# Kernel tuning notes

Hardware: AMD Instinct MI355X
Metric: run time of the kernel (lower is better)

The kernel has to match this reference:

```python
import jax, jax.numpy as jnp
import numpy as np

N_NODES = 100000
N_EDGES = 3200000
N_FEAT = 16
N_GRAPHS = 1024


def setup_inputs() -> dict:
    key = jax.random.key(0)
    ks = jax.random.split(key, 12)
    x = jax.random.normal(ks[0], (N_NODES, N_FEAT), dtype=jnp.float32)
    edge_index = jax.random.randint(ks[1], (2, N_EDGES), 0, N_NODES, dtype=jnp.int32)
    batch = jnp.sort(jax.random.randint(ks[2], (N_NODES,), 0, N_GRAPHS, dtype=jnp.int32))
    def lin(k, fan_in, fan_out):
        s = 1.0 / np.sqrt(fan_in)
        return jax.random.uniform(k, (fan_in, fan_out), jnp.float32, -s, s)
    W1 = lin(ks[3], N_FEAT, 64); b1 = jnp.zeros((64,), jnp.float32)
    W2 = lin(ks[4], 64, 32);     b2 = jnp.zeros((32,), jnp.float32)
    fc1_W = lin(ks[5], 32, 16);  fc1_b = jnp.zeros((16,), jnp.float32)
    fc2_W = lin(ks[6], 16, 1);   fc2_b = jnp.zeros((1,), jnp.float32)
    return {"x": x, "edge_index": edge_index, "batch": batch,
            "W1": W1, "b1": b1, "W2": W2, "b2": b2,
            "fc1_W": fc1_W, "fc1_b": fc1_b, "fc2_W": fc2_W, "fc2_b": fc2_b}


def _gcn_conv(h, W, b, src, dst, norm, n_nodes):
    # h: [N, Fin] -> [N, Fout]; symmetric-normalized scatter-add (PyG GCNConv)
    h = h @ W
    msg = h[src] * norm[:, None]            # edge-wise gather + scale
    out = jax.ops.segment_sum(msg, dst, num_segments=n_nodes)
    return out + b


def reference(x, edge_index, batch, W1, b1, W2, b2, fc1_W, fc1_b, fc2_W, fc2_b):
    n_nodes = x.shape[0]
    # add self-loops
    loops = jnp.arange(n_nodes, dtype=edge_index.dtype)
    src = jnp.concatenate([edge_index[0], loops])
    dst = jnp.concatenate([edge_index[1], loops])
    deg = jax.ops.segment_sum(jnp.ones_like(dst, dtype=x.dtype), dst, num_segments=n_nodes)
    dinv = jnp.where(deg > 0, jax.lax.rsqrt(deg), 0.0)
    norm = dinv[src] * dinv[dst]

    h = jax.nn.relu(_gcn_conv(x, W1, b1, src, dst, norm, n_nodes))
    # dropout p=0.2 is identity at inference
    h = jax.nn.relu(_gcn_conv(h, W2, b2, src, dst, norm, n_nodes))

    # global mean pool over graphs
    sums = jax.ops.segment_sum(h, batch, num_segments=N_GRAPHS)
    cnts = jax.ops.segment_sum(jnp.ones((n_nodes,), h.dtype), batch, num_segments=N_GRAPHS)
    g = sums / jnp.maximum(cnts, 1.0)[:, None]

    g = jax.nn.relu(g @ fc1_W + fc1_b)
    # dropout p=0.5 is identity at inference
    out = g @ fc2_W + fc2_b
    return jax.nn.sigmoid(out)  # [N_GRAPHS, 1]
```

## Files before the change

### kernel.cpp

```cpp
#include <hip/hip_runtime.h>
#include <math.h>

#define NNODES  100000
#define NEDGES  3200000
#define NGRAPHS 1024
#define BNODES  196
#define NBUCK   ((NNODES + BNODES - 1) / BNODES)
#define SCAP    12288
#define CHUNK   4096
#define NCHUNKS ((NEDGES + CHUNK - 1) / CHUNK)

typedef int iv4 __attribute__((ext_vector_type(4)));
typedef float fv2 __attribute__((ext_vector_type(2)));

#if defined(__has_builtin)
#if __has_builtin(__builtin_amdgcn_cvt_pk_f32_fp8) && __has_builtin(__builtin_amdgcn_cvt_pk_fp8_f32)
#define HW_FP8 1
#endif
#endif

__device__ __forceinline__ unsigned bf16pair(float a, float b) {
    unsigned ua = __float_as_uint(a), ub = __float_as_uint(b);
    ua += 0x7fffu + ((ua >> 16) & 1u);
    ub += 0x7fffu + ((ub >> 16) & 1u);
    return (ua >> 16) | (ub & 0xffff0000u);
}
__device__ __forceinline__ float bflo(unsigned u) { return __uint_as_float(u << 16); }
__device__ __forceinline__ float bfhi(unsigned u) { return __uint_as_float(u & 0xffff0000u); }

__device__ __forceinline__ unsigned fp8_of(float v) {
    unsigned s = (__float_as_uint(v) >> 24) & 0x80u;
    float a = fminf(fabsf(v), 448.f);
    unsigned ub = __float_as_uint(a);
    unsigned lsb = (ub >> 20) & 1u;
    ub += 0x0007FFFFu + lsb;
    int em = (int)(ub >> 20) - (120 << 3);
    if (em < 1) return s;
    if (em > 0x7E) em = 0x7E;
    return s | (unsigned)em;
}
__device__ __forceinline__ float fp8_to_f(unsigned b) {
    unsigned em = b & 0x7Fu;
    unsigned s = (b & 0x80u) << 24;
    float f = __uint_as_float(s | ((em + 0x3C0u) << 20));
    return (em >= 8u) ? f : 0.f;
}
__device__ __forceinline__ void fp8x4_to_f(unsigned w, float& f0, float& f1, float& f2, float& f3) {
#ifdef HW_FP8
    fv2 lo = __builtin_amdgcn_cvt_pk_f32_fp8((int)w, false);
    fv2 hi = __builtin_amdgcn_cvt_pk_f32_fp8((int)w, true);
    f0 = lo.x; f1 = lo.y; f2 = hi.x; f3 = hi.y;
#else
    f0 = fp8_to_f(w & 0xFFu);
    f1 = fp8_to_f((w >> 8) & 0xFFu);
    f2 = fp8_to_f((w >> 16) & 0xFFu);
    f3 = fp8_to_f(w >> 24);
#endif
}
__device__ __forceinline__ unsigned fp8x4_pack(float a, float b, float c, float d) {
    a = fminf(fmaxf(a, -448.f), 448.f);
    b = fminf(fmaxf(b, -448.f), 448.f);
    c = fminf(fmaxf(c, -448.f), 448.f);
    d = fminf(fmaxf(d, -448.f), 448.f);
#ifdef HW_FP8
    int w = __builtin_amdgcn_cvt_pk_fp8_f32(a, b, 0, false);
    w = __builtin_amdgcn_cvt_pk_fp8_f32(c, d, w, true);
    return (unsigned)w;
#else
    return fp8_of(a) | (fp8_of(b) << 8) | (fp8_of(c) << 16) | (fp8_of(d) << 24);
#endif
}


__global__ void zero4_kernel(int4* p, int nvec) {
    int i = blockIdx.x * blockDim.x + threadIdx.x;
    if (i < nvec) p[i] = make_int4(0, 0, 0, 0);
}


__global__ void binA_kernel(const int* __restrict__ src, const int* __restrict__ dst,
                            int* __restrict__ bucketCur, int* __restrict__ stage) {
    __shared__ int lcnt[NBUCK + 1];
    __shared__ int boff[NBUCK + 1];
    __shared__ int gbase[NBUCK + 1];
    __shared__ int cur[NBUCK + 1];
    __shared__ int ssum[256];
    __shared__ int packed[CHUNK];
    __shared__ unsigned short bof[CHUNK];
    int tid = threadIdx.x;
    int beg = blockIdx.x * CHUNK;
    int end = beg + CHUNK; if (end > NEDGES) end = NEDGES;
    int cnt = end - beg;

    for (int i = tid; i <= NBUCK; i += 256) lcnt[i] = 0;
    __syncthreads();

    int ent[16];
    int bk[16];
#pragma unroll
    for (int it = 0; it < 4; ++it) {
        int e0 = beg + tid * 4 + it * 1024;
        if (e0 < end) {
            iv4 d4 = __builtin_nontemporal_load((const iv4*)(dst + e0));
            iv4 s4 = __builtin_nontemporal_load((const iv4*)(src + e0));
            int b;
            b = d4.x / BNODES; ent[it*4+0] = s4.x | ((d4.x - b*BNODES) << 17); bk[it*4+0] = b; atomicAdd(&lcnt[b], 1);
            b = d4.y / BNODES; ent[it*4+1] = s4.y | ((d4.y - b*BNODES) << 17); bk[it*4+1] = b; atomicAdd(&lcnt[b], 1);
            b = d4.z / BNODES; ent[it*4+2] = s4.z | ((d4.z - b*BNODES) << 17); bk[it*4+2] = b; atomicAdd(&lcnt[b], 1);
            b = d4.w / BNODES; ent[it*4+3] = s4.w | ((d4.w - b*BNODES) << 17); bk[it*4+3] = b; atomicAdd(&lcnt[b], 1);
        } else {
            bk[it*4+0] = -1; bk[it*4+1] = -1; bk[it*4+2] = -1; bk[it*4+3] = -1;
            ent[it*4+0] = 0; ent[it*4+1] = 0; ent[it*4+2] = 0; ent[it*4+3] = 0;
        }
    }
    __syncthreads();

    int b0 = 2 * tid, b1 = 2 * tid + 1;
    int c0 = lcnt[b0];
    int c1 = (b1 < NBUCK) ? lcnt[b1] : 0;
    int sum = c0 + c1;
    ssum[tid] = sum;
    __syncthreads();
    for (int o = 1; o < 256; o <<= 1) {
        int t = (tid >= o) ? ssum[tid - o] : 0;
        __syncthreads();
        ssum[tid] += t;
        __syncthreads();
    }
    int excl = ssum[tid] - sum;
    boff[b0] = excl; cur[b0] = excl;
    if (b1 < NBUCK) { boff[b1] = excl + c0; cur[b1] = excl + c0; }
    if (c0 > 0) gbase[b0] = atomicAdd(&bucketCur[b0], c0);
    if (b1 < NBUCK && c1 > 0) gbase[b1] = atomicAdd(&bucketCur[b1], c1);
    __syncthreads();

#pragma unroll
    for (int k = 0; k < 16; ++k) {
        int b = bk[k];
        if (b >= 0) {
            int p = atomicAdd(&cur[b], 1);
            packed[p] = ent[k];
            bof[p] = (unsigned short)b;
        }
    }
    __syncthreads();

    for (int i = tid; i < cnt; i += 256) {
        int b = bof[i];
        int addr = b * SCAP + gbase[b] + (i - boff[b]);
        stage[addr] = packed[i];
    }
}


__global__ void scanE_kernel(const int* __restrict__ bucketCur, int* __restrict__ ebase) {
    int lane = threadIdx.x;
    int run = 0;
    for (int base = 0; base < NBUCK; base += 64) {
        int idx = base + lane;
        int own = (idx < NBUCK) ? bucketCur[idx] : 0;
        int v = own;
        for (int o = 1; o < 64; o <<= 1) {
            int t = __shfl_up(v, o, 64);
            if (lane >= o) v += t;
        }
        if (idx < NBUCK) ebase[idx] = run + v - own;
        run += __shfl(v, 63, 64);
    }
}


__global__ void binB_kernel(const int* __restrict__ bucketCur, const int* __restrict__ ebase,
                            const int* __restrict__ stage, const float2* __restrict__ x,
                            int* __restrict__ entries, int* __restrict__ rowptr,
                            int* __restrict__ rowend, float* __restrict__ dinv,
                            unsigned* __restrict__ xs) {
    __shared__ int s[256];
    __shared__ int ncur[256];
    __shared__ float ndinv[256];
    int b = blockIdx.x;
    int cntE = bucketCur[b];
    int eb = ebase[b];
    int nlo = b * BNODES;
    int nn = NNODES - nlo; if (nn > BNODES) nn = BNODES;
    int sb = b * SCAP;
    int tid = threadIdx.x;

    s[tid] = 0;
    __syncthreads();
    for (int e = tid; e < cntE; e += 256) {
        unsigned w = (unsigned)stage[sb + e];
        atomicAdd(&s[w >> 17], 1);
    }
    __syncthreads();
    int v = s[tid];
    for (int o = 1; o < 256; o <<= 1) {
        int t = (tid >= o) ? s[tid - o] : 0;
        __syncthreads();
        s[tid] += t;
        __syncthreads();
    }
    int excl = s[tid] - v;
    ncur[tid] = excl;
    if (tid < nn) {
        rowptr[nlo + tid] = eb + excl;
        rowend[nlo + tid] = eb + excl + v;
        float di = rsqrtf((float)(v + 1));
        dinv[nlo + tid] = di;
        ndinv[tid] = di;
    }
    __syncthreads();
    for (int i = tid; i < nn * 8; i += 256) {
        int node = i >> 3, w = i & 7;
        float2 v2 = x[(size_t)(nlo + node) * 8 + w];
        float di = ndinv[node];
        xs[(nlo + node) * 8 + w] = bf16pair(v2.x * di, v2.y * di);
    }
    for (int e = tid; e < cntE; e += 256) {
        unsigned w = (unsigned)stage[sb + e];
        int dl = w >> 17;
        int slot = atomicAdd(&ncur[dl], 1);
        entries[eb + slot] = (int)(w & 0x1FFFFu);
    }
}


__global__ void gather1_mlp_kernel(const int* __restrict__ entries, const int* __restrict__ rowptr,
                                   const int* __restrict__ rowend, const float* __restrict__ dinv,
                                   const unsigned* __restrict__ xs,
                                   const float* __restrict__ W1, const float* __restrict__ b1,
                                   const float* __restrict__ W2, unsigned* __restrict__ hm2f) {
    __shared__ float w1s[16 * 64];
    __shared__ float w2s[64 * 32];
    __shared__ float bb1[64];
    __shared__ float axs[32][17];
    __shared__ float h1s[32][65];
    int tid = threadIdx.x;
    for (int i = tid; i < 16 * 64; i += 256) w1s[i] = W1[i];
    for (int i = tid; i < 64 * 32; i += 256) w2s[i] = W2[i];
    if (tid < 64) bb1[tid] = b1[tid];

    int t = blockIdx.x * 256 + tid;
    int n = t >> 3, lane = t & 7;
    int nl = tid >> 3;
    int beg = rowptr[n], end = rowend[n];
    unsigned self = xs[n * 8 + lane];
    float a0 = bflo(self), a1 = bfhi(self);

    int base = beg;
    int m = end - base; if (m > 8) m = 8; if (m < 0) m = 0;
    int s = (lane < m) ? __builtin_nontemporal_load(entries + base + lane) : 0;
    while (base < end) {
        int nbase = base + 8;
        int nm = end - nbase; if (nm > 8) nm = 8;
        int ns = (nbase < end && lane < nm) ? __builtin_nontemporal_load(entries + nbase + lane) : 0;
        if (m == 8) {
#pragma unroll
            for (int j = 0; j < 8; ++j) {
                unsigned v = xs[__shfl(s, j, 8) * 8 + lane];
                a0 += bflo(v); a1 += bfhi(v);
            }
        } else {
            for (int j = 0; j < m; ++j) {
                unsigned v = xs[__shfl(s, j, 8) * 8 + lane];
                a0 += bflo(v); a1 += bfhi(v);
            }
        }
        s = ns; m = nm; base = nbase;
    }
    float di = dinv[n];
    axs[nl][lane * 2]     = a0 * di;
    axs[nl][lane * 2 + 1] = a1 * di;
    __syncthreads();

    {
        int j0 = lane * 8;
        float h[8];
#pragma unroll
        for (int jj = 0; jj < 8; ++jj) h[jj] = bb1[j0 + jj];
#pragma unroll
        for (int k = 0; k < 16; ++k) {
            float a = axs[nl][k];
            const float* wr = w1s + k * 64 + j0;
#pragma unroll
            for (int jj = 0; jj < 8; ++jj) h[jj] += a * wr[jj];
        }
#pragma unroll
        for (int jj = 0; jj < 8; ++jj) h1s[nl][j0 + jj] = fmaxf(h[jj], 0.f);
    }
    __syncthreads();

    {
        int j0 = lane * 4;
        float c[4] = {0.f, 0.f, 0.f, 0.f};
#pragma unroll
        for (int k = 0; k < 64; ++k) {
            float hv = h1s[nl][k];
            const float* wr = w2s + k * 32 + j0;
#pragma unroll
            for (int jj = 0; jj < 4; ++jj) c[jj] += hv * wr[jj];
        }
        float sc = di * 64.f;
        hm2f[n * 8 + lane] = fp8x4_pack(c[0] * sc, c[1] * sc, c[2] * sc, c[3] * sc);
    }
}


__global__ void gather2_pool_kernel(const int* __restrict__ entries, const int* __restrict__ rowptr,
                                    const int* __restrict__ rowend, const float* __restrict__ dinv,
                                    const unsigned* __restrict__ hm2f, const float4* __restrict__ b2,
                                    const int* __restrict__ batch,
                                    float* __restrict__ psum, float* __restrict__ pcnt) {
    __shared__ float lps[8][32];
    __shared__ float lpc[8];
    int tid = threadIdx.x;
    ((float*)lps)[tid] = 0.f;
    if (tid < 8) lpc[tid] = 0.f;

    int t = blockIdx.x * 256 + tid;
    int n = t >> 3, lane = t & 7;
    int g0 = batch[(blockIdx.x * 256) >> 3];
    int beg = rowptr[n], end = rowend[n];
    unsigned self = hm2f[n * 8 + lane];
    float a0, a1, a2, a3;
    fp8x4_to_f(self, a0, a1, a2, a3);
    __syncthreads();

    int base = beg;
    int m = end - base; if (m > 8) m = 8; if (m < 0) m = 0;
    int s = (lane < m) ? __builtin_nontemporal_load(entries + base + lane) : 0;
    while (base < end) {
        int nbase = base + 8;
        int nm = end - nbase; if (nm > 8) nm = 8;
        int ns = (nbase < end && lane < nm) ? __builtin_nontemporal_load(entries + nbase + lane) : 0;
        if (m == 8) {
#pragma unroll
            for (int j = 0; j < 8; ++j) {
                unsigned v = hm2f[__shfl(s, j, 8) * 8 + lane];
                float f0, f1, f2, f3;
                fp8x4_to_f(v, f0, f1, f2, f3);
                a0 += f0; a1 += f1; a2 += f2; a3 += f3;
            }
        } else {
            for (int j = 0; j < m; ++j) {
                unsigned v = hm2f[__shfl(s, j, 8) * 8 + lane];
                float f0, f1, f2, f3;
                fp8x4_to_f(v, f0, f1, f2, f3);
                a0 += f0; a1 += f1; a2 += f2; a3 += f3;
            }
        }
        s = ns; m = nm; base = nbase;
    }
    float sc = dinv[n] * (1.0f / 64.f);
    float4 bb = b2[lane];
    float v0 = fmaxf(a0 * sc + bb.x, 0.f);
    float v1 = fmaxf(a1 * sc + bb.y, 0.f);
    float v2 = fmaxf(a2 * sc + bb.z, 0.f);
    float v3 = fmaxf(a3 * sc + bb.w, 0.f);
    int g = batch[n];
    int gr = g - g0;
    if (gr < 8) {
        float* pg = &lps[gr][lane * 4];
        atomicAdd(pg + 0, v0);
        atomicAdd(pg + 1, v1);
        atomicAdd(pg + 2, v2);
        atomicAdd(pg + 3, v3);
        if (lane == 0) atomicAdd(&lpc[gr], 1.0f);
    } else {
        float* pg = psum + g * 32 + lane * 4;
        atomicAdd(pg + 0, v0);
        atomicAdd(pg + 1, v1);
        atomicAdd(pg + 2, v2);
        atomicAdd(pg + 3, v3);
        if (lane == 0) atomicAdd(&pcnt[g], 1.0f);
    }
    __syncthreads();
    int grf = tid >> 5, f = tid & 31;
    float v = lps[grf][f];
    if (v != 0.f) atomicAdd(&psum[(g0 + grf) * 32 + f], v);
    if (f == 0) {
        float c = lpc[grf];
        if (c != 0.f) atomicAdd(&pcnt[g0 + grf], c);
    }
}


__global__ void head_kernel(const float* __restrict__ psum, const float* __restrict__ pcnt,
                            const float* __restrict__ fc1W, const float* __restrict__ fc1b,
                            const float* __restrict__ fc2W, const float* __restrict__ fc2b,
                            float* __restrict__ out) {
    int g = blockIdx.x * blockDim.x + threadIdx.x;
    if (g >= NGRAPHS) return;
    float inv = 1.0f / fmaxf(pcnt[g], 1.0f);
    float gv[32];
#pragma unroll
    for (int k = 0; k < 32; ++k) gv[k] = psum[g * 32 + k] * inv;
    float o = fc2b[0];
#pragma unroll
    for (int j = 0; j < 16; ++j) {
        float h = fc1b[j];
#pragma unroll
        for (int k = 0; k < 32; ++k) h += gv[k] * fc1W[k * 16 + j];
        h = fmaxf(h, 0.f);
        o += h * fc2W[j];
    }
    out[g] = 1.0f / (1.0f + expf(-o));
}


extern "C" void kernel_launch(void* const* d_in, const int* in_sizes, int n_in,
                              void* d_out, int out_size, void* d_ws, size_t ws_size,
                              hipStream_t stream) {
    const float* x    = (const float*)d_in[0];
    const int*   ei   = (const int*)d_in[1];
    const int*   batch= (const int*)d_in[2];
    const float* W1   = (const float*)d_in[3];
    const float* b1   = (const float*)d_in[4];
    const float* W2   = (const float*)d_in[5];
    const float* b2   = (const float*)d_in[6];
    const float* fc1W = (const float*)d_in[7];
    const float* fc1b = (const float*)d_in[8];
    const float* fc2W = (const float*)d_in[9];
    const float* fc2b = (const float*)d_in[10];
    float* out = (float*)d_out;

    const int* src = ei;
    const int* dst = ei + NEDGES;

    char* wsb = (char*)d_ws;
    int*      bucketCur = (int*)wsb;
    float*    psum      = (float*)(wsb + 2048);
    float*    pcnt      = (float*)(wsb + 133120);
    int*      ebase     = (int*)(wsb + 137216);
    float*    dinv      = (float*)(wsb + 139264);
    int*      rowptr    = (int*)(wsb + 539264);
    int*      rowend    = (int*)(wsb + 939264);
    int*      stage     = (int*)(wsb + 1339392);
    int*      entries   = (int*)(wsb + 26456064);
    unsigned* xs        = (unsigned*)(wsb + 39256064);
    unsigned* hm2f      = (unsigned*)(wsb + 42456064);

    const int B = 256;
    zero4_kernel<<<(8576 + B - 1) / B, B, 0, stream>>>((int4*)wsb, 8576);

    binA_kernel<<<NCHUNKS, B, 0, stream>>>(src, dst, bucketCur, stage);
    scanE_kernel<<<1, 64, 0, stream>>>(bucketCur, ebase);
    binB_kernel<<<NBUCK, B, 0, stream>>>(bucketCur, ebase, stage, (const float2*)x,
                                         entries, rowptr, rowend, dinv, xs);

    gather1_mlp_kernel<<<NNODES * 8 / B, B, 0, stream>>>(entries, rowptr, rowend, dinv, xs,
                                                         W1, b1, W2, hm2f);
    gather2_pool_kernel<<<NNODES * 8 / B, B, 0, stream>>>(entries, rowptr, rowend, dinv,
                                                          hm2f, (const float4*)b2,
                                                          batch, psum, pcnt);
    head_kernel<<<(NGRAPHS + B - 1) / B, B, 0, stream>>>(psum, pcnt, fc1W, fc1b, fc2W, fc2b, out);
}
```

Before: 254.6 us.

## Remap gathers to two threads per node with 16-byte loads and split MLP

Both neighbour-gather stages now give each node two threads instead of eight. Each thread loads eight neighbour indices and issues eight independent 16-byte feature loads per iteration, which replaces the per-lane 4-byte loads and the shuffles. The layer-1 gather is split from the dense MLP into its own kernel that writes fp32 aggregates into the reused stage buffer. The MLP then reads them with float4 shared-memory accesses. This is meant to raise memory-level parallelism and cut instruction overhead in the gathers, at the cost of an extra launch, a 6.4 MB round trip through the aggregate buffer, and more work per thread on high-degree nodes.

Result: no change. 259.1 us (+1.8%).

```diff
diff --git a/kernel.cpp b/kernel.cpp
--- a/kernel.cpp
+++ b/kernel.cpp
@@ -44,18 +44,6 @@
     unsigned s = (b & 0x80u) << 24;
     float f = __uint_as_float(s | ((em + 0x3C0u) << 20));
     return (em >= 8u) ? f : 0.f;
-}
-__device__ __forceinline__ void fp8x4_to_f(unsigned w, float& f0, float& f1, float& f2, float& f3) {
-#ifdef HW_FP8
-    fv2 lo = __builtin_amdgcn_cvt_pk_f32_fp8((int)w, false);
-    fv2 hi = __builtin_amdgcn_cvt_pk_f32_fp8((int)w, true);
-    f0 = lo.x; f1 = lo.y; f2 = hi.x; f3 = hi.y;
-#else
-    f0 = fp8_to_f(w & 0xFFu);
-    f1 = fp8_to_f((w >> 8) & 0xFFu);
-    f2 = fp8_to_f((w >> 16) & 0xFFu);
-    f3 = fp8_to_f(w >> 24);
-#endif
 }
 __device__ __forceinline__ unsigned fp8x4_pack(float a, float b, float c, float d) {
     a = fminf(fmaxf(a, -448.f), 448.f);
@@ -68,6 +56,20 @@
     return (unsigned)w;
 #else
     return fp8_of(a) | (fp8_of(b) << 8) | (fp8_of(c) << 16) | (fp8_of(d) << 24);
+#endif
+}
+__device__ __forceinline__ fv2 f8lo(unsigned w) {
+#ifdef HW_FP8
+    return __builtin_amdgcn_cvt_pk_f32_fp8((int)w, false);
+#else
+    fv2 t; t.x = fp8_to_f(w & 0xFFu); t.y = fp8_to_f((w >> 8) & 0xFFu); return t;
+#endif
+}
+__device__ __forceinline__ fv2 f8hi(unsigned w) {
+#ifdef HW_FP8
+    return __builtin_amdgcn_cvt_pk_f32_fp8((int)w, true);
+#else
+    fv2 t; t.x = fp8_to_f((w >> 16) & 0xFFu); t.y = fp8_to_f(w >> 24); return t;
 #endif
 }
 
@@ -225,52 +227,87 @@
 }
 
 
-__global__ void gather1_mlp_kernel(const int* __restrict__ entries, const int* __restrict__ rowptr,
-                                   const int* __restrict__ rowend, const float* __restrict__ dinv,
-                                   const unsigned* __restrict__ xs,
-                                   const float* __restrict__ W1, const float* __restrict__ b1,
-                                   const float* __restrict__ W2, unsigned* __restrict__ hm2f) {
-    __shared__ float w1s[16 * 64];
-    __shared__ float w2s[64 * 32];
+__device__ __forceinline__ void acc_bf(unsigned u, fv2& a) {
+    fv2 t; t.x = bflo(u); t.y = bfhi(u);
+    a += t;
+}
+#define ACCX4(V) { acc_bf((V).x, acc0); acc_bf((V).y, acc1); acc_bf((V).z, acc2); acc_bf((V).w, acc3); }
+
+__global__ void __launch_bounds__(256) gatherX_kernel(const int* __restrict__ entries,
+        const int* __restrict__ rowptr, const int* __restrict__ rowend,
+        const float* __restrict__ dinv, const uint4* __restrict__ xsv,
+        float4* __restrict__ agg) {
+    int t = blockIdx.x * 256 + threadIdx.x;
+    int n = t >> 1, half = t & 1;
+    if (n >= NNODES) return;
+    int beg = rowptr[n], end = rowend[n];
+    uint4 sv = xsv[n * 2 + half];
+    fv2 acc0, acc1, acc2, acc3;
+    acc0.x = bflo(sv.x); acc0.y = bfhi(sv.x);
+    acc1.x = bflo(sv.y); acc1.y = bfhi(sv.y);
+    acc2.x = bflo(sv.z); acc2.y = bfhi(sv.z);
+    acc3.x = bflo(sv.w); acc3.y = bfhi(sv.w);
+
+    int p = beg;
+    iv4 e0 = {0,0,0,0}, e1 = {0,0,0,0};
+    bool have = (p + 8 <= end);
+    if (have) {
+        __builtin_memcpy(&e0, entries + p, 16);
+        __builtin_memcpy(&e1, entries + p + 4, 16);
+    }
+    while (have) {
+        int np = p + 8;
+        bool nhave = (np + 8 <= end);
+        iv4 f0 = e0, f1 = e1;
+        if (nhave) {
+            __builtin_memcpy(&f0, entries + np, 16);
+            __builtin_memcpy(&f1, entries + np + 4, 16);
+        }
+        uint4 v0 = xsv[e0.x * 2 + half];
+        uint4 v1 = xsv[e0.y * 2 + half];
+        uint4 v2 = xsv[e0.z * 2 + half];
+        uint4 v3 = xsv[e0.w * 2 + half];
+        uint4 v4 = xsv[e1.x * 2 + half];
+        uint4 v5 = xsv[e1.y * 2 + half];
+        uint4 v6 = xsv[e1.z * 2 + half];
+        uint4 v7 = xsv[e1.w * 2 + half];
+        ACCX4(v0); ACCX4(v1); ACCX4(v2); ACCX4(v3);
+        ACCX4(v4); ACCX4(v5); ACCX4(v6); ACCX4(v7);
+        e0 = f0; e1 = f1; p = np; have = nhave;
+    }
+    while (p < end) {
+        int e = entries[p++];
+        uint4 v = xsv[e * 2 + half];
+        ACCX4(v);
+    }
+    float di = dinv[n];
+    float4 o0, o1;
+    o0.x = acc0.x * di; o0.y = acc0.y * di; o0.z = acc1.x * di; o0.w = acc1.y * di;
+    o1.x = acc2.x * di; o1.y = acc2.y * di; o1.z = acc3.x * di; o1.w = acc3.y * di;
+    agg[n * 4 + half * 2 + 0] = o0;
+    agg[n * 4 + half * 2 + 1] = o1;
+}
+
+
+__global__ void __launch_bounds__(256) mlp_kernel(const float4* __restrict__ agg,
+        const float* __restrict__ dinv,
+        const float* __restrict__ W1, const float* __restrict__ b1,
+        const float* __restrict__ W2, unsigned* __restrict__ hm2f) {
+    __shared__ __align__(16) float w1s[16 * 64];
+    __shared__ __align__(16) float w2s[64 * 32];
     __shared__ float bb1[64];
-    __shared__ float axs[32][17];
-    __shared__ float h1s[32][65];
+    __shared__ __align__(16) float h1s[32][68];
     int tid = threadIdx.x;
     for (int i = tid; i < 16 * 64; i += 256) w1s[i] = W1[i];
     for (int i = tid; i < 64 * 32; i += 256) w2s[i] = W2[i];
     if (tid < 64) bb1[tid] = b1[tid];
 
-    int t = blockIdx.x * 256 + tid;
-    int n = t >> 3, lane = t & 7;
-    int nl = tid >> 3;
-    int beg = rowptr[n], end = rowend[n];
-    unsigned self = xs[n * 8 + lane];
-    float a0 = bflo(self), a1 = bfhi(self);
-
-    int base = beg;
-    int m = end - base; if (m > 8) m = 8; if (m < 0) m = 0;
-    int s = (lane < m) ? __builtin_nontemporal_load(entries + base + lane) : 0;
-    while (base < end) {
-        int nbase = base + 8;
-        int nm = end - nbase; if (nm > 8) nm = 8;
-        int ns = (nbase < end && lane < nm) ? __builtin_nontemporal_load(entries + nbase + lane) : 0;
-        if (m == 8) {
-#pragma unroll
-            for (int j = 0; j < 8; ++j) {
-                unsigned v = xs[__shfl(s, j, 8) * 8 + lane];
-                a0 += bflo(v); a1 += bfhi(v);
-            }
-        } else {
-            for (int j = 0; j < m; ++j) {
-                unsigned v = xs[__shfl(s, j, 8) * 8 + lane];
-                a0 += bflo(v); a1 += bfhi(v);
-            }
-        }
-        s = ns; m = nm; base = nbase;
-    }
-    float di = dinv[n];
-    axs[nl][lane * 2]     = a0 * di;
-    axs[nl][lane * 2 + 1] = a1 * di;
+    int nl = tid >> 3, lane = tid & 7;
+    int n = blockIdx.x * 32 + nl;
+    const float4* ag = agg + n * 4;
+    float4 A0 = ag[0], A1 = ag[1], A2 = ag[2], A3 = ag[3];
+    float a[16] = {A0.x, A0.y, A0.z, A0.w, A1.x, A1.y, A1.z, A1.w,
+                   A2.x, A2.y, A2.z, A2.w, A3.x, A3.y, A3.z, A3.w};
     __syncthreads();
 
     {
@@ -280,99 +317,135 @@
         for (int jj = 0; jj < 8; ++jj) h[jj] = bb1[j0 + jj];
 #pragma unroll
         for (int k = 0; k < 16; ++k) {
-            float a = axs[nl][k];
-            const float* wr = w1s + k * 64 + j0;
-#pragma unroll
-            for (int jj = 0; jj < 8; ++jj) h[jj] += a * wr[jj];
-        }
-#pragma unroll
-        for (int jj = 0; jj < 8; ++jj) h1s[nl][j0 + jj] = fmaxf(h[jj], 0.f);
+            const float4* wr = (const float4*)(w1s + k * 64 + j0);
+            float4 wa = wr[0], wb = wr[1];
+            float av = a[k];
+            h[0] += av * wa.x; h[1] += av * wa.y; h[2] += av * wa.z; h[3] += av * wa.w;
+            h[4] += av * wb.x; h[5] += av * wb.y; h[6] += av * wb.z; h[7] += av * wb.w;
+        }
+        float4 r0, r1;
+        r0.x = fmaxf(h[0], 0.f); r0.y = fmaxf(h[1], 0.f); r0.z = fmaxf(h[2], 0.f); r0.w = fmaxf(h[3], 0.f);
+        r1.x = fmaxf(h[4], 0.f); r1.y = fmaxf(h[5], 0.f); r1.z = fmaxf(h[6], 0.f); r1.w = fmaxf(h[7], 0.f);
+        float4* hw = (float4*)(&h1s[nl][j0]);
+        hw[0] = r0; hw[1] = r1;
     }
     __syncthreads();
 
     {
         int j0 = lane * 4;
-        float c[4] = {0.f, 0.f, 0.f, 0.f};
-#pragma unroll
-        for (int k = 0; k < 64; ++k) {
-            float hv = h1s[nl][k];
-            const float* wr = w2s + k * 32 + j0;
-#pragma unroll
-            for (int jj = 0; jj < 4; ++jj) c[jj] += hv * wr[jj];
-        }
-        float sc = di * 64.f;
-        hm2f[n * 8 + lane] = fp8x4_pack(c[0] * sc, c[1] * sc, c[2] * sc, c[3] * sc);
-    }
-}
-
-
-__global__ void gather2_pool_kernel(const int* __restrict__ entries, const int* __restrict__ rowptr,
-                                    const int* __restrict__ rowend, const float* __restrict__ dinv,
-                                    const unsigned* __restrict__ hm2f, const float4* __restrict__ b2,
-                                    const int* __restrict__ batch,
-                                    float* __restrict__ psum, float* __restrict__ pcnt) {
+        float c0 = 0.f, c1 = 0.f, c2 = 0.f, c3 = 0.f;
+#pragma unroll
+        for (int k = 0; k < 64; k += 4) {
+            float4 hv = *(const float4*)(&h1s[nl][k]);
+            float4 w0 = *(const float4*)(w2s + (k + 0) * 32 + j0);
+            float4 w1v = *(const float4*)(w2s + (k + 1) * 32 + j0);
+            float4 w2v = *(const float4*)(w2s + (k + 2) * 32 + j0);
+            float4 w3 = *(const float4*)(w2s + (k + 3) * 32 + j0);
+            c0 += hv.x * w0.x; c1 += hv.x * w0.y; c2 += hv.x * w0.z; c3 += hv.x * w0.w;
+            c0 += hv.y * w1v.x; c1 += hv.y * w1v.y; c2 += hv.y * w1v.z; c3 += hv.y * w1v.w;
+            c0 += hv.z * w2v.x; c1 += hv.z * w2v.y; c2 += hv.z * w2v.z; c3 += hv.z * w2v.w;
+            c0 += hv.w * w3.x; c1 += hv.w * w3.y; c2 += hv.w * w3.z; c3 += hv.w * w3.w;
+        }
+        float sc = dinv[n] * 64.f;
+        hm2f[n * 8 + lane] = fp8x4_pack(c0 * sc, c1 * sc, c2 * sc, c3 * sc);
+    }
+}
+
+
+#define ACCH4(V) { q0lo += f8lo((V).x); q0hi += f8hi((V).x); \
+                   q1lo += f8lo((V).y); q1hi += f8hi((V).y); \
+                   q2lo += f8lo((V).z); q2hi += f8hi((V).z); \
+                   q3lo += f8lo((V).w); q3hi += f8hi((V).w); }
+
+__global__ void __launch_bounds__(256) gatherH_pool_kernel(const int* __restrict__ entries,
+        const int* __restrict__ rowptr, const int* __restrict__ rowend,
+        const float* __restrict__ dinv, const uint4* __restrict__ hm4,
+        const float4* __restrict__ b2, const int* __restrict__ batch,
+        float* __restrict__ psum, float* __restrict__ pcnt) {
     __shared__ float lps[8][32];
     __shared__ float lpc[8];
     int tid = threadIdx.x;
     ((float*)lps)[tid] = 0.f;
     if (tid < 8) lpc[tid] = 0.f;
+    __syncthreads();
 
     int t = blockIdx.x * 256 + tid;
-    int n = t >> 3, lane = t & 7;
-    int g0 = batch[(blockIdx.x * 256) >> 3];
-    int beg = rowptr[n], end = rowend[n];
-    unsigned self = hm2f[n * 8 + lane];
-    float a0, a1, a2, a3;
-    fp8x4_to_f(self, a0, a1, a2, a3);
-    __syncthreads();
-
-    int base = beg;
-    int m = end - base; if (m > 8) m = 8; if (m < 0) m = 0;
-    int s = (lane < m) ? __builtin_nontemporal_load(entries + base + lane) : 0;
-    while (base < end) {
-        int nbase = base + 8;
-        int nm = end - nbase; if (nm > 8) nm = 8;
-        int ns = (nbase < end && lane < nm) ? __builtin_nontemporal_load(entries + nbase + lane) : 0;
-        if (m == 8) {
-#pragma unroll
-            for (int j = 0; j < 8; ++j) {
-                unsigned v = hm2f[__shfl(s, j, 8) * 8 + lane];
-                float f0, f1, f2, f3;
-                fp8x4_to_f(v, f0, f1, f2, f3);
-                a0 += f0; a1 += f1; a2 += f2; a3 += f3;
+    int n = t >> 1, half = t & 1;
+    int g0 = batch[(blockIdx.x * 256) >> 1];
+    if (n < NNODES) {
+        int beg = rowptr[n], end = rowend[n];
+        uint4 sv = hm4[n * 2 + half];
+        fv2 q0lo = f8lo(sv.x), q0hi = f8hi(sv.x);
+        fv2 q1lo = f8lo(sv.y), q1hi = f8hi(sv.y);
+        fv2 q2lo = f8lo(sv.z), q2hi = f8hi(sv.z);
+        fv2 q3lo = f8lo(sv.w), q3hi = f8hi(sv.w);
+
+        int p = beg;
+        iv4 e0 = {0,0,0,0}, e1 = {0,0,0,0};
+        bool have = (p + 8 <= end);
+        if (have) {
+            __builtin_memcpy(&e0, entries + p, 16);
+            __builtin_memcpy(&e1, entries + p + 4, 16);
+        }
+        while (have) {
+            int np = p + 8;
+            bool nhave = (np + 8 <= end);
+            iv4 f0 = e0, f1 = e1;
+            if (nhave) {
+                __builtin_memcpy(&f0, entries + np, 16);
+                __builtin_memcpy(&f1, entries + np + 4, 16);
             }
+            uint4 v0 = hm4[e0.x * 2 + half];
+            uint4 v1 = hm4[e0.y * 2 + half];
+            uint4 v2 = hm4[e0.z * 2 + half];
+            uint4 v3 = hm4[e0.w * 2 + half];
+            uint4 v4 = hm4[e1.x * 2 + half];
+            uint4 v5 = hm4[e1.y * 2 + half];
+            uint4 v6 = hm4[e1.z * 2 + half];
+            uint4 v7 = hm4[e1.w * 2 + half];
+            ACCH4(v0); ACCH4(v1); ACCH4(v2); ACCH4(v3);
+            ACCH4(v4); ACCH4(v5); ACCH4(v6); ACCH4(v7);
+            e0 = f0; e1 = f1; p = np; have = nhave;
+        }
+        while (p < end) {
+            int e = entries[p++];
+            uint4 v = hm4[e * 2 + half];
+            ACCH4(v);
+        }
+
+        float sc = dinv[n] * (1.0f / 64.f);
+        float4 bv0 = b2[half * 4 + 0], bv1 = b2[half * 4 + 1],
+               bv2 = b2[half * 4 + 2], bv3 = b2[half * 4 + 3];
+        float vv[16];
+        vv[0]  = fmaxf(q0lo.x * sc + bv0.x, 0.f);
+        vv[1]  = fmaxf(q0lo.y * sc + bv0.y, 0.f);
+        vv[2]  = fmaxf(q0hi.x * sc + bv0.z, 0.f);
+        vv[3]  = fmaxf(q0hi.y * sc + bv0.w, 0.f);
+        vv[4]  = fmaxf(q1lo.x * sc + bv1.x, 0.f);
+        vv[5]  = fmaxf(q1lo.y * sc + bv1.y, 0.f);
+        vv[6]  = fmaxf(q1hi.x * sc + bv1.z, 0.f);
+        vv[7]  = fmaxf(q1hi.y * sc + bv1.w, 0.f);
+        vv[8]  = fmaxf(q2lo.x * sc + bv2.x, 0.f);
+        vv[9]  = fmaxf(q2lo.y * sc + bv2.y, 0.f);
+        vv[10] = fmaxf(q2hi.x * sc + bv2.z, 0.f);
+        vv[11] = fmaxf(q2hi.y * sc + bv2.w, 0.f);
+        vv[12] = fmaxf(q3lo.x * sc + bv3.x, 0.f);
+        vv[13] = fmaxf(q3lo.y * sc + bv3.y, 0.f);
+        vv[14] = fmaxf(q3hi.x * sc + bv3.z, 0.f);
+        vv[15] = fmaxf(q3hi.y * sc + bv3.w, 0.f);
+
+        int g = batch[n], gr = g - g0;
+        if (gr < 8) {
+            float* pg = &lps[gr][half * 16];
+#pragma unroll
+            for (int k2 = 0; k2 < 16; ++k2) atomicAdd(pg + k2, vv[k2]);
+            if (half == 0) atomicAdd(&lpc[gr], 1.0f);
         } else {
-            for (int j = 0; j < m; ++j) {
-                unsigned v = hm2f[__shfl(s, j, 8) * 8 + lane];
-                float f0, f1, f2, f3;
-                fp8x4_to_f(v, f0, f1, f2, f3);
-                a0 += f0; a1 += f1; a2 += f2; a3 += f3;
-            }
-        }
-        s = ns; m = nm; base = nbase;
-    }
-    float sc = dinv[n] * (1.0f / 64.f);
-    float4 bb = b2[lane];
-    float v0 = fmaxf(a0 * sc + bb.x, 0.f);
-    float v1 = fmaxf(a1 * sc + bb.y, 0.f);
-    float v2 = fmaxf(a2 * sc + bb.z, 0.f);
-    float v3 = fmaxf(a3 * sc + bb.w, 0.f);
-    int g = batch[n];
-    int gr = g - g0;
-    if (gr < 8) {
-        float* pg = &lps[gr][lane * 4];
-        atomicAdd(pg + 0, v0);
-        atomicAdd(pg + 1, v1);
-        atomicAdd(pg + 2, v2);
-        atomicAdd(pg + 3, v3);
-        if (lane == 0) atomicAdd(&lpc[gr], 1.0f);
-    } else {
-        float* pg = psum + g * 32 + lane * 4;
-        atomicAdd(pg + 0, v0);
-        atomicAdd(pg + 1, v1);
-        atomicAdd(pg + 2, v2);
-        atomicAdd(pg + 3, v3);
-        if (lane == 0) atomicAdd(&pcnt[g], 1.0f);
+            float* pg = psum + g * 32 + half * 16;
+#pragma unroll
+            for (int k2 = 0; k2 < 16; ++k2) atomicAdd(pg + k2, vv[k2]);
+            if (half == 0) atomicAdd(&pcnt[g], 1.0f);
+        }
     }
     __syncthreads();
     int grf = tid >> 5, f = tid & 31;
@@ -439,6 +512,7 @@
     int*      entries   = (int*)(wsb + 26456064);
     unsigned* xs        = (unsigned*)(wsb + 39256064);
     unsigned* hm2f      = (unsigned*)(wsb + 42456064);
+    float4*   agg       = (float4*)(wsb + 1339392);
 
     const int B = 256;
     zero4_kernel<<<(8576 + B - 1) / B, B, 0, stream>>>((int4*)wsb, 8576);
@@ -448,10 +522,12 @@
     binB_kernel<<<NBUCK, B, 0, stream>>>(bucketCur, ebase, stage, (const float2*)x,
                                          entries, rowptr, rowend, dinv, xs);
 
-    gather1_mlp_kernel<<<NNODES * 8 / B, B, 0, stream>>>(entries, rowptr, rowend, dinv, xs,
-                                                         W1, b1, W2, hm2f);
-    gather2_pool_kernel<<<NNODES * 8 / B, B, 0, stream>>>(entries, rowptr, rowend, dinv,
-                                                          hm2f, (const float4*)b2,
-                                                          batch, psum, pcnt);
+    const int GTH = (2 * NNODES + B - 1) / B;
+    gatherX_kernel<<<GTH, B, 0, stream>>>(entries, rowptr, rowend, dinv,
+                                          (const uint4*)xs, agg);
+    mlp_kernel<<<NNODES / 32, B, 0, stream>>>((const float4*)agg, dinv, W1, b1, W2, hm2f);
+    gatherH_pool_kernel<<<GTH, B, 0, stream>>>(entries, rowptr, rowend, dinv,
+                                               (const uint4*)hm2f, (const float4*)b2,
+                                               batch, psum, pcnt);
     head_kernel<<<(NGRAPHS + B - 1) / B, B, 0, stream>>>(psum, pcnt, fc1W, fc1b, fc2W, fc2b, out);
 }
```
